# Performance work log

Measured on AMD Instinct MI355X. Metric: run time of the kernel, lower is better.

The kernel has to match this reference:

```python
import jax, jax.numpy as jnp
import numpy as np

BIN = (4, 4)
BN_EPS = 1e-5


def patch_split(t, bin_size):
    # b c (bh rh) (bw rw) -> b (bh bw) rh rw c
    B, C, H, W = t.shape
    bh, bw = bin_size
    rH, rW = H // bh, W // bw
    t = t.reshape(B, C, bh, rH, bw, rW)
    t = jnp.transpose(t, (0, 2, 4, 3, 5, 1))
    return t.reshape(B, bh * bw, rH, rW, C)


def patch_recover(t, bin_size):
    # b (bh bw) rh rw c -> b c (bh rh) (bw rw)
    B, N, rH, rW, C = t.shape
    bh, bw = bin_size
    t = t.reshape(B, bh, bw, rH, rW, C)
    t = jnp.transpose(t, (0, 5, 1, 3, 2, 4))
    return t.reshape(B, C, bh * rH, bw * rW)


def setup_inputs() -> dict:
    key = jax.random.key(0)
    ks = jax.random.split(key, 12)
    B, C, H, W = 4, 512, 128, 128
    Ci = C // 2
    bins = BIN[0] * BIN[1]
    s = lambda fan: 1.0 / np.sqrt(fan)
    return {
        "x": jax.random.normal(ks[0], (B, C, H, W), jnp.float32),
        "w_cam": jax.random.normal(ks[1], (C, C), jnp.float32) * s(C),
        "b_cam": jnp.zeros((C,), jnp.float32),
        "w_gcn1": jax.random.normal(ks[2], (bins, bins), jnp.float32) * s(bins),
        "w_gcn2": jax.random.normal(ks[3], (C, C), jnp.float32) * s(C),
        "w_fuse": jax.random.normal(ks[4], (bins,), jnp.float32) * s(bins),
        "b_fuse": jnp.zeros((1,), jnp.float32),
        "w_q": jax.random.normal(ks[5], (Ci, C), jnp.float32) * s(C),
        "b_q": jnp.zeros((Ci,), jnp.float32),
        "w_k": jax.random.normal(ks[6], (Ci, C), jnp.float32) * s(C),
        "b_k": jnp.zeros((Ci,), jnp.float32),
        "w_v": jax.random.normal(ks[7], (Ci, C), jnp.float32) * s(C),
        "b_v": jnp.zeros((Ci,), jnp.float32),
        "w_out": jax.random.normal(ks[8], (C, Ci), jnp.float32) * s(Ci),
        "bn_gamma": jnp.ones((C,), jnp.float32),
        "bn_beta": jnp.zeros((C,), jnp.float32),
        "bn_mean": jnp.zeros((C,), jnp.float32),
        "bn_var": jnp.ones((C,), jnp.float32),
    }


def reference(x, w_cam, b_cam, w_gcn1, w_gcn2, w_fuse, b_fuse,
              w_q, b_q, w_k, b_k, w_v, b_v, w_out,
              bn_gamma, bn_beta, bn_mean, bn_var):
    B, C, H, W = x.shape
    bh, bw = BIN
    bins = bh * bw
    rH, rW = H // bh, W // bw
    P = rH * rW
    K = w_cam.shape[0]  # num_classes == C

    # conv_cam: 1x1 conv (dropout is identity in eval mode)
    cam = jnp.einsum('bchw,kc->bkhw', x, w_cam) + b_cam[None, :, None, None]

    # adaptive avg pool to (bh, bw) then sigmoid
    pooled = cam.reshape(B, K, bh, rH, bw, rW).mean(axis=(3, 5))  # [B,K,bh,bw]
    cls_score = jax.nn.sigmoid(pooled)

    residual = x
    cam_p = patch_split(cam, BIN).reshape(B, bins, P, K)
    x_p = patch_split(x, BIN).reshape(B, bins, P, C)

    # bin confidence: [B, bins, K, 1]
    bin_conf = jnp.transpose(cls_score.reshape(B, K, bins), (0, 2, 1))[..., None]
    pixel_conf = jax.nn.softmax(cam_p, axis=2)  # softmax over pixels in bin

    # local_feats: [B, bins, K, C]
    local = jnp.einsum('bnpk,bnpc->bnkc', pixel_conf, x_p) * bin_conf

    # GCN over bin (node) dimension
    g = jnp.einsum('nm,bmkc->bnkc', w_gcn1, local)
    g = jax.nn.relu(g + local)
    local_feats = jnp.einsum('bnkc,dc->bnkd', g, w_gcn2)

    # fuse: 1x1 conv bins->1, relu -> global feats [B, K, C]
    glob = jnp.einsum('m,bmkc->bkc', w_fuse, local_feats) + b_fuse[0]
    glob = jax.nn.relu(glob)

    # QKV (no scale applied in original forward)
    query = jnp.einsum('bnpc,ic->bnpi', x_p, w_q) + b_q
    key_t = jnp.einsum('bnkc,ic->bnki', local_feats, w_k) + b_k
    value = jnp.einsum('bkc,ic->bki', glob, w_v) + b_v  # shared across bins

    aff = jnp.einsum('bnpi,bnki->bnpk', query, key_t)
    aff = jax.nn.softmax(aff, axis=-1)
    out = jnp.einsum('bnpk,bki->bnpi', aff, value)  # [B, bins, P, Ci]

    Ci = value.shape[-1]
    out = out.reshape(B, bins, rH, rW, Ci)
    out = patch_recover(out, BIN)  # [B, Ci, H, W]

    # conv_out: 1x1 conv (no bias) + BN (eval) + ReLU
    y = jnp.einsum('bihw,ci->bchw', out, w_out)
    inv = jax.lax.rsqrt(bn_var + BN_EPS)
    y = (y - bn_mean[None, :, None, None]) * (bn_gamma * inv)[None, :, None, None] \
        + bn_beta[None, :, None, None]
    y = jax.nn.relu(y)
    return residual + y
```

## Files before the change

### kernel.cpp

```cpp
#include <hip/hip_runtime.h>
#include <hip/hip_bf16.h>
#include <stdint.h>


typedef __attribute__((ext_vector_type(8))) short bfrag;
typedef __attribute__((ext_vector_type(4))) float ffrag;
typedef __hip_bfloat16 bf16;

__device__ __forceinline__ void load_lds16(const void* g, void* l) {
    __builtin_amdgcn_global_load_lds(
        (const __attribute__((address_space(1))) void*)(uintptr_t)g,
        (__attribute__((address_space(3))) void*)(uintptr_t)l,
        16, 0, 0);
}

template<int EPI, int GID>
__global__ void __launch_bounds__(256) gemm_bf16(
    const short* __restrict__ A, int aBatch,
    const short* __restrict__ B, int bBatch, int bShift,
    short* __restrict__ C, int cBatch,
    int M, int N, int K, int mT, int nT, int zTotal,
    const float* __restrict__ biasM, const float* __restrict__ biasN,
    const float* __restrict__ scaleM,
    const float* __restrict__ xres,
    const float* __restrict__ bng, const float* __restrict__ bnb,
    const float* __restrict__ bnm, const float* __restrict__ bnv)
{
    __shared__ char smem[32768];
    short* As = (short*)smem;
    short* Bs = (short*)(smem + 16384);
    float* eps = (float*)smem;
    const int t = threadIdx.x;
    const int w = t >> 6, lane = t & 63;

    const int id = blockIdx.x;
    const int T = mT * nT;
    int bt, mt, nt;
    if (zTotal >= 8) {
        const int x = id & 7, q = id >> 3;
        const int tile = q % T;
        bt = (q / T) * 8 + x;
        mt = tile / nT; nt = tile % nT;
    } else if (zTotal == 1 && (mT & 7) == 0) {
        const int x = id & 7, q = id >> 3;
        nt = q % nT;
        mt = x * (mT >> 3) + q / nT;
        bt = 0;
    } else {
        bt = id / T;
        const int tile = id % T;
        mt = tile / nT; nt = tile % nT;
    }
    const int m0 = mt * 128, n0 = nt * 128;

    const short* gA = A + (size_t)bt * aBatch;
    const short* gB = B + (size_t)(bt >> bShift) * bBatch;
    const int wm = w >> 1, wn = w & 1;

    ffrag acc[4][4] = {};

    const int rowbase = w * 32;
    const int lr = lane >> 3;
    const int lc = lane & 7;

    for (int k0 = 0; k0 < K; k0 += 64) {
#pragma unroll
        for (int j = 0; j < 4; ++j) {
            const int rr = rowbase + j * 8 + lr;
            const int ch = lc ^ (rr & 7);
            load_lds16(gA + (size_t)(m0 + rr) * K + k0 + ch * 8,
                       &As[(rowbase + j * 8) * 64]);
            load_lds16(gB + (size_t)(n0 + rr) * K + k0 + ch * 8,
                       &Bs[(rowbase + j * 8) * 64]);
        }
        __syncthreads();
#pragma unroll
        for (int kk = 0; kk < 2; ++kk) {
            bfrag af[4], bfv[4];
#pragma unroll
            for (int i = 0; i < 4; ++i) {
                const int ra = wm * 64 + i * 16 + (lane & 15);
                const int cl = kk * 4 + (lane >> 4);
                af[i]  = *(const bfrag*)&As[ra * 64 + ((cl ^ (ra & 7)) * 8)];
                const int rb = wn * 64 + i * 16 + (lane & 15);
                bfv[i] = *(const bfrag*)&Bs[rb * 64 + ((cl ^ (rb & 7)) * 8)];
            }
#pragma unroll
            for (int i = 0; i < 4; ++i)
#pragma unroll
                for (int j = 0; j < 4; ++j)
                    acc[i][j] = __builtin_amdgcn_mfma_f32_16x16x32_bf16(
                        af[i], bfv[j], acc[i][j], 0, 0, 0);
        }
        __syncthreads();
    }

    if (EPI == 0) {
        bf16* gC = (bf16*)(C + (size_t)bt * cBatch);
#pragma unroll
        for (int i = 0; i < 4; ++i) {
#pragma unroll
            for (int j = 0; j < 4; ++j) {
                const int col = n0 + wn * 64 + j * 16 + (lane & 15);
                const float bnvl = biasN ? biasN[col] : 0.f;
#pragma unroll
                for (int r = 0; r < 4; ++r) {
                    const int row = m0 + wm * 64 + i * 16 + (lane >> 4) * 4 + r;
                    float v = acc[i][j][r] + bnvl + (biasM ? biasM[row] : 0.f);
                    if (scaleM) v *= scaleM[bt * M + row];
                    gC[(size_t)row * N + col] = __float2bfloat16(v);
                }
            }
        }
    } else {
        float* O = (float*)C;
        const int b = bt >> 4, binq = bt & 15;
        const int h0 = (binq >> 2) * 32, w0q = (binq & 3) * 32;
        const int l4 = lane >> 4, l15 = lane & 15;
        const int rho = t >> 3, col0 = (t & 7) * 16;
#pragma unroll
        for (int i = 0; i < 4; ++i) {
            if (i) __syncthreads();
#pragma unroll
            for (int j = 0; j < 4; ++j)
#pragma unroll
                for (int r = 0; r < 4; ++r)
                    eps[(wm * 16 + 4 * l4 + r) * 133 + wn * 64 + j * 16 + l15]
                        = acc[i][j][r];
            __syncthreads();
            const int c = m0 + (rho >> 4) * 64 + i * 16 + (rho & 15);
            const float sc = bng[c] * rsqrtf(bnv[c] + 1e-5f);
            const float mm = bnm[c], bb = bnb[c];
#pragma unroll
            for (int u = 0; u < 4; ++u) {
                const int p = n0 + col0 + u * 4;
                const size_t flat =
                    (((size_t)b * 512 + c) * 128 + h0 + (p >> 5)) * 128
                    + w0q + (p & 31);
                const float4 q4 = *(const float4*)&eps[rho * 133 + col0 + u * 4];
                const float4 xr = *(const float4*)&xres[flat];
                float4 o;
                o.x = xr.x + fmaxf(fmaf(q4.x - mm, sc, bb), 0.f);
                o.y = xr.y + fmaxf(fmaf(q4.y - mm, sc, bb), 0.f);
                o.z = xr.z + fmaxf(fmaf(q4.z - mm, sc, bb), 0.f);
                o.w = xr.w + fmaxf(fmaf(q4.w - mm, sc, bb), 0.f);
                *(float4*)&O[flat] = o;
            }
        }
    }
}

__global__ void __launch_bounds__(256) wconv(
    const float* __restrict__ wc, const float* __restrict__ wg2,
    const float* __restrict__ wq, const float* __restrict__ wk,
    const float* __restrict__ wv, const float* __restrict__ wo,
    bf16* __restrict__ dst)
{
    const int i = blockIdx.x * 256 + threadIdx.x;
    const float* s; int o;
    if      (i <  262144) { s = wc;  o = i; }
    else if (i <  524288) { s = wg2; o = i - 262144; }
    else if (i <  655360) { s = wq;  o = i - 524288; }
    else if (i <  786432) { s = wk;  o = i - 655360; }
    else if (i <  917504) { s = wv;  o = i - 786432; }
    else                  { s = wo;  o = i - 917504; }
    dst[i] = __float2bfloat16(s[o]);
}

__global__ void __launch_bounds__(256) convert_x(
    const float* __restrict__ x, bf16* __restrict__ xpc, bf16* __restrict__ xcp)
{
    const int bn = blockIdx.x, ct = blockIdx.y, ph = blockIdx.z;
    const int b = bn >> 4, n = bn & 15;
    const int c0 = ct * 64;
    const int h0 = (n >> 2) * 32 + ph * 2;
    const int w0 = (n & 3) * 32;
    const int P0 = ph * 64;
    __shared__ float tile[64][65];
    const int t = threadIdx.x;

#pragma unroll
    for (int r = 0; r < 4; ++r) {
        const int flat = r * 1024 + t * 4;
        const int ci = flat >> 6;
        const int p  = flat & 63;
        const float4 v = *(const float4*)
            &x[(((size_t)b * 512 + c0 + ci) * 128 + h0 + (p >> 5)) * 128
               + w0 + (p & 31)];
        *(float4*)&tile[ci][p] = v;
        bf16 tmp[4];
        tmp[0] = __float2bfloat16(v.x);
        tmp[1] = __float2bfloat16(v.y);
        tmp[2] = __float2bfloat16(v.z);
        tmp[3] = __float2bfloat16(v.w);
        *(uint2*)&xcp[((size_t)bn * 512 + c0 + ci) * 1024 + P0 + p] =
            *(const uint2*)tmp;
    }
    __syncthreads();

    {
        const int pi = t >> 2;
        const int cb = (t & 3) * 16;
        bf16 tmp[16];
#pragma unroll
        for (int j = 0; j < 16; ++j)
            tmp[j] = __float2bfloat16(tile[cb + j][pi]);
        bf16* dst = &xpc[((size_t)bn * 1024 + P0 + pi) * 512 + c0 + cb];
        *(bfrag*)dst       = *(const bfrag*)&tmp[0];
        *(bfrag*)(dst + 8) = *(const bfrag*)&tmp[8];
    }
}

__global__ void __launch_bounds__(256) softmax_pool_1024(
    bf16* __restrict__ conf, float* __restrict__ binconf)
{
    const int row = blockIdx.x;
    bf16* r = conf + (size_t)row * 1024;
    const int t = threadIdx.x;
    bf16 a[4];
    *(uint2*)a = *(const uint2*)(r + t * 4);
    float f[4];
#pragma unroll
    for (int i = 0; i < 4; ++i) f[i] = __bfloat162float(a[i]);
    float s  = f[0] + f[1] + f[2] + f[3];
    float mx = fmaxf(fmaxf(f[0], f[1]), fmaxf(f[2], f[3]));
#pragma unroll
    for (int off = 32; off > 0; off >>= 1) {
        s += __shfl_down(s, off, 64);
        mx = fmaxf(mx, __shfl_down(mx, off, 64));
    }
    __shared__ float rs[4], rm[4], re[4];
    const int wv = t >> 6, ln = t & 63;
    if (ln == 0) { rs[wv] = s; rm[wv] = mx; }
    __syncthreads();
    const float MX = fmaxf(fmaxf(rm[0], rm[1]), fmaxf(rm[2], rm[3]));
    if (t == 0) {
        const float mean = (rs[0] + rs[1] + rs[2] + rs[3]) * (1.f / 1024.f);
        binconf[row] = 1.f / (1.f + __expf(-mean));
    }
    float e[4];
#pragma unroll
    for (int i = 0; i < 4; ++i) e[i] = __expf(f[i] - MX);
    float es = e[0] + e[1] + e[2] + e[3];
#pragma unroll
    for (int off = 32; off > 0; off >>= 1) es += __shfl_down(es, off, 64);
    if (ln == 0) re[wv] = es;
    __syncthreads();
    const float inv = 1.f / (re[0] + re[1] + re[2] + re[3]);
#pragma unroll
    for (int i = 0; i < 4; ++i) a[i] = __float2bfloat16(e[i] * inv);
    *(uint2*)(r + t * 4) = *(uint2*)a;
}

__global__ void __launch_bounds__(256) softmax_rows_512(bf16* __restrict__ aff)
{
    const int t = threadIdx.x;
    const int wv = t >> 6, ln = t & 63;
    const int row = blockIdx.x * 4 + wv;
    bf16* r = aff + (size_t)row * 512;
    bf16 a[8];
    *(uint4*)a = *(const uint4*)(r + ln * 8);
    float f[8];
#pragma unroll
    for (int i = 0; i < 8; ++i) f[i] = __bfloat162float(a[i]);
    float mx = f[0];
#pragma unroll
    for (int i = 1; i < 8; ++i) mx = fmaxf(mx, f[i]);
#pragma unroll
    for (int off = 32; off > 0; off >>= 1) mx = fmaxf(mx, __shfl_down(mx, off, 64));
    mx = __shfl(mx, 0, 64);
    float es = 0.f;
#pragma unroll
    for (int i = 0; i < 8; ++i) { f[i] = __expf(f[i] - mx); es += f[i]; }
#pragma unroll
    for (int off = 32; off > 0; off >>= 1) es += __shfl_down(es, off, 64);
    es = __shfl(es, 0, 64);
    const float inv = 1.f / es;
#pragma unroll
    for (int i = 0; i < 8; ++i) a[i] = __float2bfloat16(f[i] * inv);
    *(uint4*)(r + ln * 8) = *(uint4*)a;
}

__global__ void __launch_bounds__(256) gcn1_kernel(
    const bf16* __restrict__ localb, bf16* __restrict__ g,
    const float* __restrict__ w_gcn1)
{
    __shared__ float wsm[16][16];
    const int t = threadIdx.x;
    wsm[t >> 4][t & 15] = w_gcn1[t];
    const int idx = blockIdx.x * 256 + t;
    const int b  = idx >> 18;
    const int kc = idx & 262143;
    const bf16* lp = localb + (size_t)b * 4194304 + kc;
    __syncthreads();
    float lv[16];
#pragma unroll
    for (int m = 0; m < 16; ++m) lv[m] = __bfloat162float(lp[m * 262144]);
    bf16* gp = g + (size_t)b * 4194304 + kc;
#pragma unroll
    for (int n = 0; n < 16; ++n) {
        float acc = lv[n];
#pragma unroll
        for (int m = 0; m < 16; ++m) acc = fmaf(wsm[n][m], lv[m], acc);
        gp[n * 262144] = __float2bfloat16(fmaxf(acc, 0.f));
    }
}

__global__ void __launch_bounds__(256) glob_kernel(
    const bf16* __restrict__ lfeats, bf16* __restrict__ glob,
    const float* __restrict__ w_fuse, const float* __restrict__ b_fuse)
{
    const int idx = blockIdx.x * 256 + threadIdx.x;
    const int b  = idx >> 18;
    const int kc = idx & 262143;
    const bf16* lp = lfeats + (size_t)b * 4194304 + kc;
    float acc = b_fuse[0];
#pragma unroll
    for (int m = 0; m < 16; ++m)
        acc = fmaf(w_fuse[m], __bfloat162float(lp[m * 262144]), acc);
    glob[idx] = __float2bfloat16(fmaxf(acc, 0.f));
}

extern "C" void kernel_launch(void* const* d_in, const int* in_sizes, int n_in,
                              void* d_out, int out_size, void* d_ws, size_t ws_size,
                              hipStream_t stream) {
    (void)in_sizes; (void)n_in; (void)out_size; (void)ws_size;
    const float* x      = (const float*)d_in[0];
    const float* w_cam  = (const float*)d_in[1];
    const float* b_cam  = (const float*)d_in[2];
    const float* w_gcn1 = (const float*)d_in[3];
    const float* w_gcn2 = (const float*)d_in[4];
    const float* w_fuse = (const float*)d_in[5];
    const float* b_fuse = (const float*)d_in[6];
    const float* w_q    = (const float*)d_in[7];
    const float* b_q    = (const float*)d_in[8];
    const float* w_k    = (const float*)d_in[9];
    const float* b_k    = (const float*)d_in[10];
    const float* w_v    = (const float*)d_in[11];
    const float* b_v    = (const float*)d_in[12];
    const float* w_out  = (const float*)d_in[13];
    const float* bng    = (const float*)d_in[14];
    const float* bnb    = (const float*)d_in[15];
    const float* bnm    = (const float*)d_in[16];
    const float* bnv    = (const float*)d_in[17];

    char* base = (char*)d_ws;
    bf16*  wbf    = (bf16*)(base);
    float* bc     = (float*)(base + 2097152);
    bf16*  xpc    = (bf16*)(base + 2228224);
    bf16*  xcp    = (bf16*)(base + 69337088);
    bf16*  confb  = (bf16*)(base + 136445952);
    bf16*  localb = (bf16*)(base + 203554816);
    bf16*  g      = xcp;
    bf16*  lf     = (bf16*)(base + 102891520);
    bf16*  globb  = confb;
    bf16*  vt     = (bf16*)(base + 138543104);
    bf16*  key    = (bf16*)(base + 139067392);
    bf16*  query  = (bf16*)(base + 155844608);
    bf16*  aff    = xpc;
    bf16*  attn   = lf;

    bf16* wcam = wbf;
    bf16* wg2  = wbf + 262144;
    bf16* wq   = wbf + 524288;
    bf16* wk   = wbf + 655360;
    bf16* wv   = wbf + 786432;
    bf16* wo   = wbf + 917504;

    wconv<<<4096, 256, 0, stream>>>(w_cam, w_gcn2, w_q, w_k, w_v, w_out, wbf);
    convert_x<<<dim3(64, 8, 16), 256, 0, stream>>>(x, xpc, xcp);

    gemm_bf16<0, 1><<<4 * 8 * 64, 256, 0, stream>>>(
        (const short*)wcam, 0, (const short*)xpc, 524288, 0,
        (short*)confb, 524288, 512, 1024, 512, 4, 8, 64,
        b_cam, nullptr, nullptr, nullptr, nullptr, nullptr, nullptr, nullptr);
    softmax_pool_1024<<<32768, 256, 0, stream>>>(confb, bc);
    gemm_bf16<0, 3><<<4 * 4 * 64, 256, 0, stream>>>(
        (const short*)confb, 524288, (const short*)xcp, 524288, 0,
        (short*)localb, 262144, 512, 512, 1024, 4, 4, 64,
        nullptr, nullptr, bc, nullptr, nullptr, nullptr, nullptr, nullptr);
    gcn1_kernel<<<4096, 256, 0, stream>>>(localb, g, w_gcn1);
    gemm_bf16<0, 5><<<256 * 4, 256, 0, stream>>>(
        (const short*)g, 0, (const short*)wg2, 0, 0,
        (short*)lf, 0, 32768, 512, 512, 256, 4, 1,
        nullptr, nullptr, nullptr, nullptr, nullptr, nullptr, nullptr, nullptr);
    glob_kernel<<<4096, 256, 0, stream>>>(lf, globb, w_fuse, b_fuse);
    gemm_bf16<0, 7><<<2 * 4 * 4, 256, 0, stream>>>(
        (const short*)wv, 0, (const short*)globb, 262144, 0,
        (short*)vt, 131072, 256, 512, 512, 2, 4, 4,
        b_v, nullptr, nullptr, nullptr, nullptr, nullptr, nullptr, nullptr);
    gemm_bf16<0, 8><<<256 * 2, 256, 0, stream>>>(
        (const short*)lf, 0, (const short*)wk, 0, 0,
        (short*)key, 0, 32768, 256, 512, 256, 2, 1,
        nullptr, b_k, nullptr, nullptr, nullptr, nullptr, nullptr, nullptr);
    gemm_bf16<0, 9><<<8 * 2 * 64, 256, 0, stream>>>(
        (const short*)xpc, 524288, (const short*)wq, 0, 0,
        (short*)query, 262144, 1024, 256, 512, 8, 2, 64,
        nullptr, b_q, nullptr, nullptr, nullptr, nullptr, nullptr, nullptr);
    gemm_bf16<0, 10><<<8 * 4 * 64, 256, 0, stream>>>(
        (const short*)query, 262144, (const short*)key, 131072, 0,
        (short*)aff, 524288, 1024, 512, 256, 8, 4, 64,
        nullptr, nullptr, nullptr, nullptr, nullptr, nullptr, nullptr, nullptr);
    softmax_rows_512<<<16384, 256, 0, stream>>>(aff);
    gemm_bf16<0, 12><<<8 * 2 * 64, 256, 0, stream>>>(
        (const short*)aff, 524288, (const short*)vt, 131072, 4,
        (short*)attn, 262144, 1024, 256, 512, 8, 2, 64,
        nullptr, nullptr, nullptr, nullptr, nullptr, nullptr, nullptr, nullptr);
    gemm_bf16<1, 13><<<4 * 8 * 64, 256, 0, stream>>>(
        (const short*)wo, 0, (const short*)attn, 262144, 0,
        (short*)d_out, 0, 512, 1024, 256, 4, 8, 64,
        nullptr, nullptr, nullptr, x, bng, bnb, bnm, bnv);
}
```

Measured before the change: 773.9 us.

## Double-buffer LDS tiles in bf16 GEMM to overlap global loads with MFMA

Splits the shared-memory A/B tiles into two buffers and prefetches the next K-slice with direct global-to-LDS loads while the current slice is consumed by MFMA. Explicit vmcnt/lgkmcnt waits and raw s_barrier calls replace the plain __syncthreads pair. The aim is to hide global memory latency inside the main loop. LDS use doubles to 64KB per block, which can lower occupancy, and the epilogue scratch now aliases buffer 0.

Result: slower. 896.1 us (+15.8%).

```diff
diff --git a/kernel.cpp b/kernel.cpp
--- a/kernel.cpp
+++ b/kernel.cpp
@@ -26,10 +26,8 @@
     const float* __restrict__ bng, const float* __restrict__ bnb,
     const float* __restrict__ bnm, const float* __restrict__ bnv)
 {
-    __shared__ char smem[32768];
-    short* As = (short*)smem;
-    short* Bs = (short*)(smem + 16384);
-    float* eps = (float*)smem;
+    __shared__ short As[2][128 * 64];
+    __shared__ short Bs[2][128 * 64];
     const int t = threadIdx.x;
     const int w = t >> 6, lane = t & 63;
 
@@ -63,17 +61,30 @@
     const int lr = lane >> 3;
     const int lc = lane & 7;
 
-    for (int k0 = 0; k0 < K; k0 += 64) {
+    auto STAGE = [&](int buf, int k0) {
 #pragma unroll
         for (int j = 0; j < 4; ++j) {
             const int rr = rowbase + j * 8 + lr;
             const int ch = lc ^ (rr & 7);
             load_lds16(gA + (size_t)(m0 + rr) * K + k0 + ch * 8,
-                       &As[(rowbase + j * 8) * 64]);
+                       &As[buf][(rowbase + j * 8) * 64]);
             load_lds16(gB + (size_t)(n0 + rr) * K + k0 + ch * 8,
-                       &Bs[(rowbase + j * 8) * 64]);
+                       &Bs[buf][(rowbase + j * 8) * 64]);
         }
-        __syncthreads();
+    };
+
+    const int nK = K >> 6;
+    STAGE(0, 0);
+    for (int ks = 0; ks < nK; ++ks) {
+        const int cur = ks & 1;
+        if (ks + 1 < nK) {
+            STAGE(cur ^ 1, (ks + 1) << 6);
+            asm volatile("s_waitcnt vmcnt(8)" ::: "memory");
+        } else {
+            asm volatile("s_waitcnt vmcnt(0)" ::: "memory");
+        }
+        __builtin_amdgcn_sched_barrier(0);
+        __builtin_amdgcn_s_barrier();
 #pragma unroll
         for (int kk = 0; kk < 2; ++kk) {
             bfrag af[4], bfv[4];
@@ -81,9 +92,11 @@
             for (int i = 0; i < 4; ++i) {
                 const int ra = wm * 64 + i * 16 + (lane & 15);
                 const int cl = kk * 4 + (lane >> 4);
-                af[i]  = *(const bfrag*)&As[ra * 64 + ((cl ^ (ra & 7)) * 8)];
+                af[i]  = *(const bfrag*)
+                    &As[cur][ra * 64 + ((cl ^ (ra & 7)) * 8)];
                 const int rb = wn * 64 + i * 16 + (lane & 15);
-                bfv[i] = *(const bfrag*)&Bs[rb * 64 + ((cl ^ (rb & 7)) * 8)];
+                bfv[i] = *(const bfrag*)
+                    &Bs[cur][rb * 64 + ((cl ^ (rb & 7)) * 8)];
             }
 #pragma unroll
             for (int i = 0; i < 4; ++i)
@@ -92,7 +105,9 @@
                     acc[i][j] = __builtin_amdgcn_mfma_f32_16x16x32_bf16(
                         af[i], bfv[j], acc[i][j], 0, 0, 0);
         }
-        __syncthreads();
+        asm volatile("s_waitcnt lgkmcnt(0)" ::: "memory");
+        __builtin_amdgcn_sched_barrier(0);
+        __builtin_amdgcn_s_barrier();
     }
 
     if (EPI == 0) {
@@ -113,6 +128,7 @@
             }
         }
     } else {
+        float* eps = (float*)&As[0][0];
         float* O = (float*)C;
         const int b = bt >> 4, binq = bt & 15;
         const int h0 = (binq >> 2) * 32, w0q = (binq & 3) * 32;
```
